# Kernel tuning notes

Hardware: AMD Instinct MI355X
Metric: run time of the kernel (lower is better)

The kernel has to match this reference:

```python
import jax, jax.numpy as jnp
import numpy as np
import math

D_MODEL = 1024
N_HEADS = 16
D_HEAD = 64
D_MLP = 4096
INIT_RANGE = 0.02
VAR_EPS = 1e-05
BATCH = 2
SEQ = 2048


def new_gelu(x):
    c = math.sqrt(2.0 / math.pi)
    return 0.5 * x * (1.0 + jnp.tanh(c * (x + 0.044715 * x ** 3)))


def layer_norm(x, w, b):
    mean = jnp.mean(x, axis=-1, keepdims=True)
    x = x - mean
    var = jnp.mean(x * x, axis=-1, keepdims=True)
    return x / jnp.sqrt(var + VAR_EPS) * w + b


def setup_inputs() -> dict:
    key = jax.random.key(0)
    ks = jax.random.split(key, 12)
    s = INIT_RANGE
    return {
        "resid": jax.random.normal(ks[0], (BATCH, SEQ, D_MODEL), jnp.float32),
        "w_q": s * jax.random.normal(ks[1], (N_HEADS, D_MODEL, D_HEAD), jnp.float32),
        "w_k": s * jax.random.normal(ks[2], (N_HEADS, D_MODEL, D_HEAD), jnp.float32),
        "w_v": s * jax.random.normal(ks[3], (N_HEADS, D_MODEL, D_HEAD), jnp.float32),
        "w_o": s * jax.random.normal(ks[4], (N_HEADS, D_HEAD, D_MODEL), jnp.float32),
        "ln1_w": s * jax.random.normal(ks[5], (D_MODEL,), jnp.float32),
        "ln1_b": jnp.zeros((D_MODEL,), jnp.float32),
        "ln2_w": s * jax.random.normal(ks[6], (D_MODEL,), jnp.float32),
        "ln2_b": jnp.zeros((D_MODEL,), jnp.float32),
        "w_in": s * jax.random.normal(ks[7], (D_MODEL, D_MLP), jnp.float32),
        "b_in": jnp.zeros((D_MLP,), jnp.float32),
        "w_out": s * jax.random.normal(ks[8], (D_MLP, D_MODEL), jnp.float32),
        "b_out": jnp.zeros((D_MODEL,), jnp.float32),
    }


def attention(x, w_q, w_k, w_v, w_o):
    # x: [b, s, d]; weights: [h, d, dh] / [h, dh, d]
    qs = jnp.einsum('bsd,hde->bhse', x, w_q)
    ks = jnp.einsum('bsd,hde->bhse', x, w_k)
    vs = jnp.einsum('bsd,hde->bhse', x, w_v)
    attn = jnp.einsum('bhqe,bhke->bhqk', qs, ks)  # [b, h, s, s]
    s = attn.shape[-1]
    causal = jnp.triu(jnp.ones((s, s), dtype=bool), k=1)
    attn = jnp.where(causal, -jnp.inf, attn)
    attn = jax.nn.softmax(attn / math.sqrt(D_HEAD), axis=-1)
    z = jnp.einsum('bhqk,bhke->bhqe', attn, vs)
    return jnp.einsum('bhse,hed->bsd', z, w_o)


def reference(resid, w_q, w_k, w_v, w_o, ln1_w, ln1_b, ln2_w, ln2_b, w_in, b_in, w_out, b_out):
    resid = resid + attention(layer_norm(resid, ln1_w, ln1_b), w_q, w_k, w_v, w_o)
    h = layer_norm(resid, ln2_w, ln2_b)
    h = new_gelu(jnp.einsum('bsd,dm->bsm', h, w_in) + b_in)
    resid = resid + jnp.einsum('bsm,md->bsd', h, w_out) + b_out
    return resid
```

## Files before the change

### kernel.cpp

```cpp
#include <hip/hip_runtime.h>

#define DEV static __device__ __forceinline__

typedef unsigned short u16;
typedef __attribute__((ext_vector_type(8))) __bf16 bf16x8;
typedef __attribute__((ext_vector_type(4))) float f32x4;

DEV float bf2f(u16 u) { union { unsigned int i; float f; } v; v.i = ((unsigned int)u) << 16; return v.f; }
DEV u16 f2bf(float f) {
  union { float f; unsigned int i; } v; v.f = f;
  unsigned int r = v.i + 0x7fffu + ((v.i >> 16) & 1u);
  return (u16)(r >> 16);
}

DEV float gelu_f(float x) {
  float u = 0.7978845608028654f * (x + 0.044715f * x * x * x);
  float e = __expf(2.f * u);
  float t = 1.f - 2.f / (e + 1.f);
  return 0.5f * x * (1.f + t);
}

DEV void async16(const u16* g, u16* l) {
  __builtin_amdgcn_global_load_lds(
      (const __attribute__((address_space(1))) unsigned int*)g,
      (__attribute__((address_space(3))) unsigned int*)l, 16, 0, 0);
}

__global__ __launch_bounds__(256) void transpose_all(
    const float* __restrict__ w_q, const float* __restrict__ w_k,
    const float* __restrict__ w_v, const float* __restrict__ w_o,
    const float* __restrict__ w_in, const float* __restrict__ w_out,
    u16* __restrict__ WQKVT, u16* __restrict__ WOT,
    u16* __restrict__ WINT, u16* __restrict__ WOUTT)
{
  int t = blockIdx.x;
  const float* src; u16* dst; int R, C, c0, r0;
  if (t < 3072) {
    int seg = t >> 10, tt = t & 1023;
    int z = tt >> 6, rem = tt & 63;
    const float* w = seg == 0 ? w_q : (seg == 1 ? w_k : w_v);
    src = w + z * 65536;
    dst = WQKVT + seg * 1048576 + z * 65536;
    R = 1024; C = 64;
    c0 = (rem >> 5) * 32; r0 = (rem & 31) * 32;
  } else if (t < 4096) {
    int tt = t - 3072;
    src = w_o; dst = WOT; R = 1024; C = 1024;
    c0 = (tt & 31) * 32; r0 = (tt >> 5) * 32;
  } else if (t < 8192) {
    int tt = t - 4096;
    src = w_in; dst = WINT; R = 1024; C = 4096;
    c0 = (tt & 127) * 32; r0 = (tt >> 7) * 32;
  } else {
    int tt = t - 8192;
    src = w_out; dst = WOUTT; R = 4096; C = 1024;
    c0 = (tt & 31) * 32; r0 = (tt >> 5) * 32;
  }
  __shared__ float tile[32][33];
  int tx = threadIdx.x & 31, ty = threadIdx.x >> 5;
#pragma unroll
  for (int i = 0; i < 32; i += 8)
    tile[ty + i][tx] = src[(size_t)(r0 + ty + i) * C + (c0 + tx)];
  __syncthreads();
#pragma unroll
  for (int i = 0; i < 32; i += 8)
    dst[(size_t)(c0 + ty + i) * R + (r0 + tx)] = f2bf(tile[tx][ty + i]);
}

__global__ __launch_bounds__(256) void ln_kernel(
    const float* __restrict__ x, const float* __restrict__ g,
    const float* __restrict__ b, u16* __restrict__ out)
{
  int row = blockIdx.x, tid = threadIdx.x;
  const float4 v = ((const float4*)(x + (size_t)row * 1024))[tid];
  float s = v.x + v.y + v.z + v.w;
  float ss = v.x * v.x + v.y * v.y + v.z * v.z + v.w * v.w;
#pragma unroll
  for (int m = 1; m < 64; m <<= 1) { s += __shfl_xor(s, m, 64); ss += __shfl_xor(ss, m, 64); }
  __shared__ float red[8];
  if ((tid & 63) == 0) { red[tid >> 6] = s; red[4 + (tid >> 6)] = ss; }
  __syncthreads();
  s = red[0] + red[1] + red[2] + red[3];
  ss = red[4] + red[5] + red[6] + red[7];
  float mean = s * (1.f / 1024.f);
  float var = ss * (1.f / 1024.f) - mean * mean;
  float rstd = rsqrtf(var + 1e-5f);
  float4 gv = ((const float4*)g)[tid];
  float4 bv = ((const float4*)b)[tid];
  u16* o = out + (size_t)row * 1024 + tid * 4;
  o[0] = f2bf((v.x - mean) * rstd * gv.x + bv.x);
  o[1] = f2bf((v.y - mean) * rstd * gv.y + bv.y);
  o[2] = f2bf((v.z - mean) * rstd * gv.z + bv.z);
  o[3] = f2bf((v.w - mean) * rstd * gv.w + bv.w);
}

template <int EPI, int BM, int BN>
__global__ __launch_bounds__(256) void gemm_bf16(
    const u16* __restrict__ A, const u16* __restrict__ Bt, int K, int N,
    const float* __restrict__ addv, const float* __restrict__ bias,
    float* __restrict__ outF, u16* __restrict__ o0, u16* __restrict__ o1,
    u16* __restrict__ o2)
{
  constexpr int IM = BM / 32, IN = BN / 32;
  __shared__ u16 lA[BM * 64];
  __shared__ u16 lB[BN * 64];
  const int tid = threadIdx.x;
  const int lane = tid & 63, wave = tid >> 6;
  const int wm = wave >> 1, wn = wave & 1;
  const int quad = lane >> 4, l16 = lane & 15;
  const int m0 = blockIdx.y * BM, n0 = blockIdx.x * BN;

  f32x4 acc[IM][IN] = {};

  const int srow = lane >> 3;
  const int soff = ((lane & 7) ^ srow) << 3;

  for (int kt = 0; kt < K; kt += 64) {
    __syncthreads();
#pragma unroll
    for (int q = 0; q < BM / 32; ++q) {
      int rbase = wave * (BM / 4) + q * 8;
      async16(A + (size_t)(m0 + rbase + srow) * K + kt + soff, lA + rbase * 64);
    }
#pragma unroll
    for (int q = 0; q < BN / 32; ++q) {
      int rbase = wave * (BN / 4) + q * 8;
      async16(Bt + (size_t)(n0 + rbase + srow) * K + kt + soff, lB + rbase * 64);
    }
    __syncthreads();
#pragma unroll
    for (int kk = 0; kk < 2; ++kk) {
      bf16x8 af[IM], bfr[IN];
#pragma unroll
      for (int i = 0; i < IM; ++i) {
        int ar = wm * (BM / 2) + i * 16 + l16;
        af[i] = *(const bf16x8*)&lA[ar * 64 + ((((kk * 4) + quad) ^ (ar & 7)) << 3)];
      }
#pragma unroll
      for (int j = 0; j < IN; ++j) {
        int br = wn * (BN / 2) + j * 16 + l16;
        bfr[j] = *(const bf16x8*)&lB[br * 64 + ((((kk * 4) + quad) ^ (br & 7)) << 3)];
      }
#pragma unroll
      for (int i = 0; i < IM; ++i)
#pragma unroll
        for (int j = 0; j < IN; ++j)
          acc[i][j] = __builtin_amdgcn_mfma_f32_16x16x32_bf16(af[i], bfr[j], acc[i][j], 0, 0, 0);
    }
  }

#pragma unroll
  for (int i = 0; i < IM; ++i) {
    const int rowb = m0 + wm * (BM / 2) + i * 16 + quad * 4;
#pragma unroll
    for (int j = 0; j < IN; ++j) {
      const int col = n0 + wn * (BN / 2) + j * 16 + l16;
#pragma unroll
      for (int rr = 0; rr < 4; ++rr) {
        const int m = rowb + rr;
        const float v = acc[i][j][rr];
        if (EPI == 0) {
          int bb = m >> 11, s = m & 2047;
          int proj = col >> 10, hc = col & 1023, hh = hc >> 6, e = hc & 63;
          size_t bhh = (size_t)(bb * 16 + hh);
          if (proj == 0) o0[(bhh * 2048 + s) * 64 + e] = f2bf(v * 0.125f);
          else if (proj == 1) o1[(bhh * 2048 + s) * 64 + e] = f2bf(v);
          else o2[bhh * 131072 + (size_t)e * 2048 + s] = f2bf(v);
        } else if (EPI == 1) {
          size_t idx = (size_t)m * N + col;
          outF[idx] = v + addv[idx];
        } else if (EPI == 2) {
          o0[(size_t)m * N + col] = f2bf(gelu_f(v + bias[col]));
        } else {
          size_t idx = (size_t)m * N + col;
          outF[idx] = v + bias[col] + addv[idx];
        }
      }
    }
  }
}

__global__ __launch_bounds__(256) void attn_flash(
    const u16* __restrict__ Q, const u16* __restrict__ K,
    const u16* __restrict__ Vt, u16* __restrict__ Z)
{
  __shared__ u16 lK[64 * 64];
  __shared__ u16 lV[64 * 64];
  __shared__ u16 lP[4][16 * 64];

  const int tid = threadIdx.x;
  const int lane = tid & 63, wave = tid >> 6;
  const int quad = lane >> 4, l16 = lane & 15;

  const int flat = blockIdx.x;
  const int xcd = flat & 7, w = flat >> 3;
  const int bhid = xcd * 4 + (w >> 5);
  const int qtile = 31 - (w & 31);
  const int b = bhid >> 4, h = bhid & 15;
  const size_t bh = (size_t)bhid;
  const int q0b = qtile * 64;
  const int q0w = q0b + wave * 16;

  const int srow = lane >> 3;
  const int soff = ((lane & 7) ^ srow) << 3;

  bf16x8 qf[2];
#pragma unroll
  for (int d = 0; d < 2; ++d)
    qf[d] = *(const bf16x8*)(Q + (bh * 2048 + (size_t)(q0w + l16)) * 64 + d * 32 + quad * 8);

  f32x4 oacc[4] = {};
  float lrow[4] = {};

  u16* myP = lP[wave];
  const int kend = q0b + 64;

  for (int kt0 = 0; kt0 < kend; kt0 += 64) {
    __syncthreads();
#pragma unroll
    for (int q = 0; q < 2; ++q) {
      int rbase = wave * 16 + q * 8;
      async16(K + (bh * 2048 + (size_t)(kt0 + rbase + srow)) * 64 + soff, lK + rbase * 64);
      async16(Vt + bh * 131072 + (size_t)(rbase + srow) * 2048 + kt0 + soff, lV + rbase * 64);
    }
    __syncthreads();

    bf16x8 kf[4][2];
#pragma unroll
    for (int j = 0; j < 4; ++j)
#pragma unroll
      for (int d = 0; d < 2; ++d) {
        int key = j * 16 + l16;
        kf[j][d] = *(const bf16x8*)(lK + key * 64 + (((d * 4 + quad) ^ (key & 7)) << 3));
      }
    f32x4 sv[4];
#pragma unroll
    for (int j = 0; j < 4; ++j) {
      f32x4 z = {};
      z = __builtin_amdgcn_mfma_f32_16x16x32_bf16(qf[0], kf[j][0], z, 0, 0, 0);
      z = __builtin_amdgcn_mfma_f32_16x16x32_bf16(qf[1], kf[j][1], z, 0, 0, 0);
      sv[j] = z;
    }

    const bool needMask = (kt0 + 63 > q0w);
#pragma unroll
    for (int rr = 0; rr < 4; ++rr) {
      int rowl = quad * 4 + rr;
      int rowg = q0w + rowl;
      u16* prow = myP + rowl * 64;
      float accl = lrow[rr];
#pragma unroll
      for (int j = 0; j < 4; ++j) {
        float p = __expf(sv[j][rr]);
        if (needMask && (kt0 + j * 16 + l16 > rowg)) p = 0.f;
        accl += p;
        int chk = j * 2 + (l16 >> 3);
        prow[((chk ^ (rowl & 7)) << 3) + (l16 & 7)] = (u16)(__float_as_uint(p) >> 16);
      }
      lrow[rr] = accl;
    }

#pragma unroll
    for (int ks = 0; ks < 2; ++ks) {
      int chk = ks * 4 + quad;
      bf16x8 pf, vf[4];
      pf = *(const bf16x8*)(myP + l16 * 64 + ((chk ^ (l16 & 7)) << 3));
#pragma unroll
      for (int d = 0; d < 4; ++d) {
        int dh = d * 16 + l16;
        vf[d] = *(const bf16x8*)(lV + dh * 64 + ((chk ^ (dh & 7)) << 3));
      }
#pragma unroll
      for (int d = 0; d < 4; ++d)
        oacc[d] = __builtin_amdgcn_mfma_f32_16x16x32_bf16(pf, vf[d], oacc[d], 0, 0, 0);
    }
  }

#pragma unroll
  for (int rr = 0; rr < 4; ++rr) {
    float l = lrow[rr];
#pragma unroll
    for (int msk = 1; msk < 16; msk <<= 1) l += __shfl_xor(l, msk, 64);
    lrow[rr] = 1.f / l;
  }
#pragma unroll
  for (int d = 0; d < 4; ++d)
#pragma unroll
    for (int rr = 0; rr < 4; ++rr) {
      int srowq = q0w + quad * 4 + rr;
      Z[((size_t)(b * 2048 + srowq)) * 1024 + h * 64 + d * 16 + l16] =
          f2bf(oacc[d][rr] * lrow[rr]);
    }
}

extern "C" void kernel_launch(void* const* d_in, const int* in_sizes, int n_in,
                              void* d_out, int out_size, void* d_ws, size_t ws_size,
                              hipStream_t stream) {
  const float* resid = (const float*)d_in[0];
  const float* w_q  = (const float*)d_in[1];
  const float* w_k  = (const float*)d_in[2];
  const float* w_v  = (const float*)d_in[3];
  const float* w_o  = (const float*)d_in[4];
  const float* ln1w = (const float*)d_in[5];
  const float* ln1b = (const float*)d_in[6];
  const float* ln2w = (const float*)d_in[7];
  const float* ln2b = (const float*)d_in[8];
  const float* w_in = (const float*)d_in[9];
  const float* b_in = (const float*)d_in[10];
  const float* w_out= (const float*)d_in[11];
  const float* b_out= (const float*)d_in[12];
  float* out = (float*)d_out;

  const size_t MB = 1u << 20;
  char* ws = (char*)d_ws;
  u16* WQKVT = (u16*)(ws + 0);
  u16* WOT   = (u16*)(ws + 6 * MB);
  u16* WINT  = (u16*)(ws + 8 * MB);
  u16* WOUTT = (u16*)(ws + 16 * MB);
  u16* X1    = (u16*)(ws + 24 * MB);
  u16* Qb    = (u16*)(ws + 32 * MB);
  u16* Kb    = (u16*)(ws + 40 * MB);
  u16* Vb    = (u16*)(ws + 48 * MB);
  u16* Zb    = (u16*)(ws + 56 * MB);
  float* R2  = (float*)(ws + 64 * MB);
  u16* Hb    = (u16*)(ws + 80 * MB);
  u16* Gb    = (u16*)(ws + 24 * MB);

  transpose_all<<<dim3(12288), 256, 0, stream>>>(w_q, w_k, w_v, w_o, w_in, w_out,
                                                 WQKVT, WOT, WINT, WOUTT);
  ln_kernel<<<4096, 256, 0, stream>>>(resid, ln1w, ln1b, X1);
  gemm_bf16<0, 64, 128><<<dim3(24, 64), 256, 0, stream>>>(X1, WQKVT, 1024, 3072, nullptr, nullptr, nullptr, Qb, Kb, Vb);
  attn_flash<<<dim3(1024), 256, 0, stream>>>(Qb, Kb, Vb, Zb);
  gemm_bf16<1, 64, 64><<<dim3(16, 64), 256, 0, stream>>>(Zb, WOT, 1024, 1024, resid, nullptr, R2, nullptr, nullptr, nullptr);
  ln_kernel<<<4096, 256, 0, stream>>>(R2, ln2w, ln2b, Hb);
  gemm_bf16<2, 64, 128><<<dim3(32, 64), 256, 0, stream>>>(Hb, WINT, 1024, 4096, nullptr, b_in, nullptr, Gb, nullptr, nullptr);
  gemm_bf16<3, 64, 64><<<dim3(16, 64), 256, 0, stream>>>(Gb, WOUTT, 4096, 1024, R2, b_out, out, nullptr, nullptr, nullptr);
}
```

Before: 372.5 us.

## Load GEMM and attention operands directly from global memory, bypassing LDS staging

New measurement: 657.8 us. +76.6%, slower.

```diff
diff --git a/kernel.cpp b/kernel.cpp
--- a/kernel.cpp
+++ b/kernel.cpp
@@ -94,67 +94,50 @@
   o[3] = f2bf((v.w - mean) * rstd * gv.w + bv.w);
 }
 
-template <int EPI, int BM, int BN>
-__global__ __launch_bounds__(256) void gemm_bf16(
+template <int EPI>
+__global__ __launch_bounds__(256, 3) void gemm_direct(
     const u16* __restrict__ A, const u16* __restrict__ Bt, int K, int N,
-    const float* __restrict__ addv, const float* __restrict__ bias,
-    float* __restrict__ outF, u16* __restrict__ o0, u16* __restrict__ o1,
-    u16* __restrict__ o2)
-{
-  constexpr int IM = BM / 32, IN = BN / 32;
-  __shared__ u16 lA[BM * 64];
-  __shared__ u16 lB[BN * 64];
+    int nPerXcd, const float* __restrict__ bias,
+    u16* __restrict__ o0, u16* __restrict__ o1, u16* __restrict__ o2)
+{
   const int tid = threadIdx.x;
   const int lane = tid & 63, wave = tid >> 6;
   const int wm = wave >> 1, wn = wave & 1;
   const int quad = lane >> 4, l16 = lane & 15;
-  const int m0 = blockIdx.y * BM, n0 = blockIdx.x * BN;
-
-  f32x4 acc[IM][IN] = {};
-
-  const int srow = lane >> 3;
-  const int soff = ((lane & 7) ^ srow) << 3;
-
-  for (int kt = 0; kt < K; kt += 64) {
-    __syncthreads();
-#pragma unroll
-    for (int q = 0; q < BM / 32; ++q) {
-      int rbase = wave * (BM / 4) + q * 8;
-      async16(A + (size_t)(m0 + rbase + srow) * K + kt + soff, lA + rbase * 64);
-    }
-#pragma unroll
-    for (int q = 0; q < BN / 32; ++q) {
-      int rbase = wave * (BN / 4) + q * 8;
-      async16(Bt + (size_t)(n0 + rbase + srow) * K + kt + soff, lB + rbase * 64);
-    }
-    __syncthreads();
-#pragma unroll
-    for (int kk = 0; kk < 2; ++kk) {
-      bf16x8 af[IM], bfr[IN];
-#pragma unroll
-      for (int i = 0; i < IM; ++i) {
-        int ar = wm * (BM / 2) + i * 16 + l16;
-        af[i] = *(const bf16x8*)&lA[ar * 64 + ((((kk * 4) + quad) ^ (ar & 7)) << 3)];
-      }
-#pragma unroll
-      for (int j = 0; j < IN; ++j) {
-        int br = wn * (BN / 2) + j * 16 + l16;
-        bfr[j] = *(const bf16x8*)&lB[br * 64 + ((((kk * 4) + quad) ^ (br & 7)) << 3)];
-      }
-#pragma unroll
-      for (int i = 0; i < IM; ++i)
-#pragma unroll
-        for (int j = 0; j < IN; ++j)
-          acc[i][j] = __builtin_amdgcn_mfma_f32_16x16x32_bf16(af[i], bfr[j], acc[i][j], 0, 0, 0);
-    }
-  }
-
-#pragma unroll
-  for (int i = 0; i < IM; ++i) {
-    const int rowb = m0 + wm * (BM / 2) + i * 16 + quad * 4;
-#pragma unroll
-    for (int j = 0; j < IN; ++j) {
-      const int col = n0 + wn * (BN / 2) + j * 16 + l16;
+
+  const int id = blockIdx.x;
+  const int xcd = id & 7, slot = id >> 3;
+  const int n_t = xcd * nPerXcd + slot % nPerXcd;
+  const int m_t = slot / nPerXcd;
+  const int m0 = m_t * 128, n0 = n_t * 128;
+
+  f32x4 acc[4][4] = {};
+
+  const u16* Abase = A + (size_t)(m0 + wm * 64 + l16) * K + quad * 8;
+  const u16* Bbase = Bt + (size_t)(n0 + wn * 64 + l16) * K + quad * 8;
+
+#pragma unroll 2
+  for (int kt = 0; kt < K; kt += 32) {
+    bf16x8 af[4], bf[4];
+#pragma unroll
+    for (int i = 0; i < 4; ++i)
+      af[i] = *(const bf16x8*)(Abase + (size_t)(i * 16) * K + kt);
+#pragma unroll
+    for (int j = 0; j < 4; ++j)
+      bf[j] = *(const bf16x8*)(Bbase + (size_t)(j * 16) * K + kt);
+#pragma unroll
+    for (int i = 0; i < 4; ++i)
+#pragma unroll
+      for (int j = 0; j < 4; ++j)
+        acc[i][j] = __builtin_amdgcn_mfma_f32_16x16x32_bf16(af[i], bf[j], acc[i][j], 0, 0, 0);
+  }
+
+#pragma unroll
+  for (int i = 0; i < 4; ++i) {
+    const int rowb = m0 + wm * 64 + i * 16 + quad * 4;
+#pragma unroll
+    for (int j = 0; j < 4; ++j) {
+      const int col = n0 + wn * 64 + j * 16 + l16;
 #pragma unroll
       for (int rr = 0; rr < 4; ++rr) {
         const int m = rowb + rr;
@@ -166,15 +149,81 @@
           if (proj == 0) o0[(bhh * 2048 + s) * 64 + e] = f2bf(v * 0.125f);
           else if (proj == 1) o1[(bhh * 2048 + s) * 64 + e] = f2bf(v);
           else o2[bhh * 131072 + (size_t)e * 2048 + s] = f2bf(v);
-        } else if (EPI == 1) {
-          size_t idx = (size_t)m * N + col;
-          outF[idx] = v + addv[idx];
-        } else if (EPI == 2) {
+        } else {
           o0[(size_t)m * N + col] = f2bf(gelu_f(v + bias[col]));
-        } else {
-          size_t idx = (size_t)m * N + col;
-          outF[idx] = v + bias[col] + addv[idx];
         }
+      }
+    }
+  }
+}
+
+template <int EPI, int BM, int BN>
+__global__ __launch_bounds__(256) void gemm_bf16(
+    const u16* __restrict__ A, const u16* __restrict__ Bt, int K, int N,
+    const float* __restrict__ addv, const float* __restrict__ bias,
+    float* __restrict__ outF)
+{
+  constexpr int IM = BM / 32, IN = BN / 32;
+  __shared__ u16 lA[BM * 64];
+  __shared__ u16 lB[BN * 64];
+  const int tid = threadIdx.x;
+  const int lane = tid & 63, wave = tid >> 6;
+  const int wm = wave >> 1, wn = wave & 1;
+  const int quad = lane >> 4, l16 = lane & 15;
+  const int m0 = blockIdx.y * BM, n0 = blockIdx.x * BN;
+
+  f32x4 acc[IM][IN] = {};
+
+  const int srow = lane >> 3;
+  const int soff = ((lane & 7) ^ srow) << 3;
+
+  for (int kt = 0; kt < K; kt += 64) {
+    __syncthreads();
+#pragma unroll
+    for (int q = 0; q < BM / 32; ++q) {
+      int rbase = wave * (BM / 4) + q * 8;
+      async16(A + (size_t)(m0 + rbase + srow) * K + kt + soff, lA + rbase * 64);
+    }
+#pragma unroll
+    for (int q = 0; q < BN / 32; ++q) {
+      int rbase = wave * (BN / 4) + q * 8;
+      async16(Bt + (size_t)(n0 + rbase + srow) * K + kt + soff, lB + rbase * 64);
+    }
+    __syncthreads();
+#pragma unroll
+    for (int kk = 0; kk < 2; ++kk) {
+      bf16x8 af[IM], bfr[IN];
+#pragma unroll
+      for (int i = 0; i < IM; ++i) {
+        int ar = wm * (BM / 2) + i * 16 + l16;
+        af[i] = *(const bf16x8*)&lA[ar * 64 + ((((kk * 4) + quad) ^ (ar & 7)) << 3)];
+      }
+#pragma unroll
+      for (int j = 0; j < IN; ++j) {
+        int br = wn * (BN / 2) + j * 16 + l16;
+        bfr[j] = *(const bf16x8*)&lB[br * 64 + ((((kk * 4) + quad) ^ (br & 7)) << 3)];
+      }
+#pragma unroll
+      for (int i = 0; i < IM; ++i)
+#pragma unroll
+        for (int j = 0; j < IN; ++j)
+          acc[i][j] = __builtin_amdgcn_mfma_f32_16x16x32_bf16(af[i], bfr[j], acc[i][j], 0, 0, 0);
+    }
+  }
+
+#pragma unroll
+  for (int i = 0; i < IM; ++i) {
+    const int rowb = m0 + wm * (BM / 2) + i * 16 + quad * 4;
+#pragma unroll
+    for (int j = 0; j < IN; ++j) {
+      const int col = n0 + wn * (BN / 2) + j * 16 + l16;
+#pragma unroll
+      for (int rr = 0; rr < 4; ++rr) {
+        const int m = rowb + rr;
+        const float v = acc[i][j][rr];
+        size_t idx = (size_t)m * N + col;
+        if (EPI == 1) outF[idx] = v + addv[idx];
+        else          outF[idx] = v + bias[col] + addv[idx];
       }
     }
   }
@@ -184,8 +233,6 @@
     const u16* __restrict__ Q, const u16* __restrict__ K,
     const u16* __restrict__ Vt, u16* __restrict__ Z)
 {
-  __shared__ u16 lK[64 * 64];
-  __shared__ u16 lV[64 * 64];
   __shared__ u16 lP[4][16 * 64];
 
   const int tid = threadIdx.x;
@@ -201,9 +248,6 @@
   const int q0b = qtile * 64;
   const int q0w = q0b + wave * 16;
 
-  const int srow = lane >> 3;
-  const int soff = ((lane & 7) ^ srow) << 3;
-
   bf16x8 qf[2];
 #pragma unroll
   for (int d = 0; d < 2; ++d)
@@ -214,25 +258,23 @@
 
   u16* myP = lP[wave];
   const int kend = q0b + 64;
+  const u16* Kb = K + bh * 2048 * 64;
+  const u16* Vb = Vt + bh * 131072;
 
   for (int kt0 = 0; kt0 < kend; kt0 += 64) {
-    __syncthreads();
-#pragma unroll
-    for (int q = 0; q < 2; ++q) {
-      int rbase = wave * 16 + q * 8;
-      async16(K + (bh * 2048 + (size_t)(kt0 + rbase + srow)) * 64 + soff, lK + rbase * 64);
-      async16(Vt + bh * 131072 + (size_t)(rbase + srow) * 2048 + kt0 + soff, lV + rbase * 64);
-    }
-    __syncthreads();
-
     bf16x8 kf[4][2];
 #pragma unroll
     for (int j = 0; j < 4; ++j)
 #pragma unroll
-      for (int d = 0; d < 2; ++d) {
-        int key = j * 16 + l16;
-        kf[j][d] = *(const bf16x8*)(lK + key * 64 + (((d * 4 + quad) ^ (key & 7)) << 3));
-      }
+      for (int d = 0; d < 2; ++d)
+        kf[j][d] = *(const bf16x8*)(Kb + (size_t)(kt0 + j * 16 + l16) * 64 + d * 32 + quad * 8);
+    bf16x8 vf[2][4];
+#pragma unroll
+    for (int ks = 0; ks < 2; ++ks)
+#pragma unroll
+      for (int d = 0; d < 4; ++d)
+        vf[ks][d] = *(const bf16x8*)(Vb + (size_t)(d * 16 + l16) * 2048 + kt0 + ks * 32 + quad * 8);
+
     f32x4 sv[4];
 #pragma unroll
     for (int j = 0; j < 4; ++j) {
@@ -263,16 +305,10 @@
 #pragma unroll
     for (int ks = 0; ks < 2; ++ks) {
       int chk = ks * 4 + quad;
-      bf16x8 pf, vf[4];
-      pf = *(const bf16x8*)(myP + l16 * 64 + ((chk ^ (l16 & 7)) << 3));
-#pragma unroll
-      for (int d = 0; d < 4; ++d) {
-        int dh = d * 16 + l16;
-        vf[d] = *(const bf16x8*)(lV + dh * 64 + ((chk ^ (dh & 7)) << 3));
-      }
+      bf16x8 pf = *(const bf16x8*)(myP + l16 * 64 + ((chk ^ (l16 & 7)) << 3));
 #pragma unroll
       for (int d = 0; d < 4; ++d)
-        oacc[d] = __builtin_amdgcn_mfma_f32_16x16x32_bf16(pf, vf[d], oacc[d], 0, 0, 0);
+        oacc[d] = __builtin_amdgcn_mfma_f32_16x16x32_bf16(pf, vf[ks][d], oacc[d], 0, 0, 0);
     }
   }
 
@@ -329,10 +365,10 @@
   transpose_all<<<dim3(12288), 256, 0, stream>>>(w_q, w_k, w_v, w_o, w_in, w_out,
                                                  WQKVT, WOT, WINT, WOUTT);
   ln_kernel<<<4096, 256, 0, stream>>>(resid, ln1w, ln1b, X1);
-  gemm_bf16<0, 64, 128><<<dim3(24, 64), 256, 0, stream>>>(X1, WQKVT, 1024, 3072, nullptr, nullptr, nullptr, Qb, Kb, Vb);
+  gemm_direct<0><<<dim3(768), 256, 0, stream>>>(X1, WQKVT, 1024, 3072, 3, nullptr, Qb, Kb, Vb);
   attn_flash<<<dim3(1024), 256, 0, stream>>>(Qb, Kb, Vb, Zb);
-  gemm_bf16<1, 64, 64><<<dim3(16, 64), 256, 0, stream>>>(Zb, WOT, 1024, 1024, resid, nullptr, R2, nullptr, nullptr, nullptr);
+  gemm_bf16<1, 64, 64><<<dim3(16, 64), 256, 0, stream>>>(Zb, WOT, 1024, 1024, resid, nullptr, R2);
   ln_kernel<<<4096, 256, 0, stream>>>(R2, ln2w, ln2b, Hb);
-  gemm_bf16<2, 64, 128><<<dim3(32, 64), 256, 0, stream>>>(Hb, WINT, 1024, 4096, nullptr, b_in, nullptr, Gb, nullptr, nullptr);
-  gemm_bf16<3, 64, 64><<<dim3(16, 64), 256, 0, stream>>>(Gb, WOUTT, 4096, 1024, R2, b_out, out, nullptr, nullptr, nullptr);
-}
+  gemm_direct<2><<<dim3(1024), 256, 0, stream>>>(Hb, WINT, 1024, 4096, 4, b_in, Gb, nullptr, nullptr);
+  gemm_bf16<3, 64, 64><<<dim3(16, 64), 256, 0, stream>>>(Gb, WOUTT, 4096, 1024, R2, b_out, out);
+}
```

## Double-buffer K/V tiles in flash attention and XCD-swizzle GEMM tile mapping

Applied to the files above, without the earlier changes.

Result: no change. 379.2 us (+1.8%).

```diff
diff --git a/kernel.cpp b/kernel.cpp
--- a/kernel.cpp
+++ b/kernel.cpp
@@ -97,7 +97,7 @@
 template <int EPI, int BM, int BN>
 __global__ __launch_bounds__(256) void gemm_bf16(
     const u16* __restrict__ A, const u16* __restrict__ Bt, int K, int N,
-    const float* __restrict__ addv, const float* __restrict__ bias,
+    int nPerXcd, const float* __restrict__ addv, const float* __restrict__ bias,
     float* __restrict__ outF, u16* __restrict__ o0, u16* __restrict__ o1,
     u16* __restrict__ o2)
 {
@@ -108,7 +108,12 @@
   const int lane = tid & 63, wave = tid >> 6;
   const int wm = wave >> 1, wn = wave & 1;
   const int quad = lane >> 4, l16 = lane & 15;
-  const int m0 = blockIdx.y * BM, n0 = blockIdx.x * BN;
+
+  const int id = blockIdx.x;
+  const int xcd = id & 7, slot = id >> 3;
+  const int n_t = xcd * nPerXcd + slot % nPerXcd;
+  const int m_t = slot / nPerXcd;
+  const int m0 = m_t * BM, n0 = n_t * BN;
 
   f32x4 acc[IM][IN] = {};
 
@@ -184,8 +189,8 @@
     const u16* __restrict__ Q, const u16* __restrict__ K,
     const u16* __restrict__ Vt, u16* __restrict__ Z)
 {
-  __shared__ u16 lK[64 * 64];
-  __shared__ u16 lV[64 * 64];
+  __shared__ u16 lK[2][64 * 64];
+  __shared__ u16 lV[2][64 * 64];
   __shared__ u16 lP[4][16 * 64];
 
   const int tid = threadIdx.x;
@@ -213,17 +218,33 @@
   float lrow[4] = {};
 
   u16* myP = lP[wave];
-  const int kend = q0b + 64;
-
-  for (int kt0 = 0; kt0 < kend; kt0 += 64) {
+  const int niter = qtile + 1;
+  const u16* Kb = K + bh * 2048 * 64;
+  const u16* Vb = Vt + bh * 131072;
+
+#pragma unroll
+  for (int q = 0; q < 2; ++q) {
+    int rbase = wave * 16 + q * 8;
+    async16(Kb + (size_t)(rbase + srow) * 64 + soff, lK[0] + rbase * 64);
+    async16(Vb + (size_t)(rbase + srow) * 2048 + soff, lV[0] + rbase * 64);
+  }
+
+  for (int it = 0; it < niter; ++it) {
     __syncthreads();
-#pragma unroll
-    for (int q = 0; q < 2; ++q) {
-      int rbase = wave * 16 + q * 8;
-      async16(K + (bh * 2048 + (size_t)(kt0 + rbase + srow)) * 64 + soff, lK + rbase * 64);
-      async16(Vt + bh * 131072 + (size_t)(rbase + srow) * 2048 + kt0 + soff, lV + rbase * 64);
-    }
-    __syncthreads();
+    const int kt0 = it << 6;
+    if (it + 1 < niter) {
+      const int kn = kt0 + 64;
+      u16* bK = lK[(it + 1) & 1];
+      u16* bV = lV[(it + 1) & 1];
+#pragma unroll
+      for (int q = 0; q < 2; ++q) {
+        int rbase = wave * 16 + q * 8;
+        async16(Kb + (size_t)(kn + rbase + srow) * 64 + soff, bK + rbase * 64);
+        async16(Vb + (size_t)(rbase + srow) * 2048 + kn + soff, bV + rbase * 64);
+      }
+    }
+    const u16* cK = lK[it & 1];
+    const u16* cV = lV[it & 1];
 
     bf16x8 kf[4][2];
 #pragma unroll
@@ -231,7 +252,7 @@
 #pragma unroll
       for (int d = 0; d < 2; ++d) {
         int key = j * 16 + l16;
-        kf[j][d] = *(const bf16x8*)(lK + key * 64 + (((d * 4 + quad) ^ (key & 7)) << 3));
+        kf[j][d] = *(const bf16x8*)(cK + key * 64 + (((d * 4 + quad) ^ (key & 7)) << 3));
       }
     f32x4 sv[4];
 #pragma unroll
@@ -268,7 +289,7 @@
 #pragma unroll
       for (int d = 0; d < 4; ++d) {
         int dh = d * 16 + l16;
-        vf[d] = *(const bf16x8*)(lV + dh * 64 + ((chk ^ (dh & 7)) << 3));
+        vf[d] = *(const bf16x8*)(cV + dh * 64 + ((chk ^ (dh & 7)) << 3));
       }
 #pragma unroll
       for (int d = 0; d < 4; ++d)
@@ -329,10 +350,10 @@
   transpose_all<<<dim3(12288), 256, 0, stream>>>(w_q, w_k, w_v, w_o, w_in, w_out,
                                                  WQKVT, WOT, WINT, WOUTT);
   ln_kernel<<<4096, 256, 0, stream>>>(resid, ln1w, ln1b, X1);
-  gemm_bf16<0, 64, 128><<<dim3(24, 64), 256, 0, stream>>>(X1, WQKVT, 1024, 3072, nullptr, nullptr, nullptr, Qb, Kb, Vb);
+  gemm_bf16<0, 64, 128><<<dim3(1536), 256, 0, stream>>>(X1, WQKVT, 1024, 3072, 3, nullptr, nullptr, nullptr, Qb, Kb, Vb);
   attn_flash<<<dim3(1024), 256, 0, stream>>>(Qb, Kb, Vb, Zb);
-  gemm_bf16<1, 64, 64><<<dim3(16, 64), 256, 0, stream>>>(Zb, WOT, 1024, 1024, resid, nullptr, R2, nullptr, nullptr, nullptr);
+  gemm_bf16<1, 64, 64><<<dim3(1024), 256, 0, stream>>>(Zb, WOT, 1024, 1024, 2, resid, nullptr, R2, nullptr, nullptr, nullptr);
   ln_kernel<<<4096, 256, 0, stream>>>(R2, ln2w, ln2b, Hb);
-  gemm_bf16<2, 64, 128><<<dim3(32, 64), 256, 0, stream>>>(Hb, WINT, 1024, 4096, nullptr, b_in, nullptr, Gb, nullptr, nullptr);
-  gemm_bf16<3, 64, 64><<<dim3(16, 64), 256, 0, stream>>>(Gb, WOUTT, 4096, 1024, R2, b_out, out, nullptr, nullptr, nullptr);
-}
+  gemm_bf16<2, 64, 128><<<dim3(2048), 256, 0, stream>>>(Hb, WINT, 1024, 4096, 4, nullptr, b_in, nullptr, Gb, nullptr, nullptr);
+  gemm_bf16<3, 64, 64><<<dim3(1024), 256, 0, stream>>>(Gb, WOUTT, 4096, 1024, 2, R2, b_out, out, nullptr, nullptr, nullptr);
+}
```
